# Kernel optimization log

Measured on AMD Instinct MI355X. Metric: run time of the kernel, lower is better.

## Reference

```python
import jax, jax.numpy as jnp
import numpy as np

B, R, A, L, P = 1024, 512, 196, 2, 4  # batch, rnn_size, att_size, num_layers, num_parallels


def setup_inputs() -> dict:
    key = jax.random.key(0)
    ks = jax.random.split(key, 24)
    s = 0.02
    inp = {
        'x': jax.random.normal(ks[0], (B, R), jnp.float32),
        'att': jax.random.normal(ks[1], (B, A, R), jnp.float32),
        'inputs': jax.random.normal(ks[2], (2 * L, B, R), jnp.float32),
        # first attention block
        'Wa2a': jax.random.normal(ks[3], (A, R), jnp.float32) * s,
        'ba2a': jnp.zeros((A,), jnp.float32),
        'Wh2a': jax.random.normal(ks[4], (A, R), jnp.float32) * s,
        'bh2a': jnp.zeros((A,), jnp.float32),
        'Wd2d': jax.random.normal(ks[5], (1, A), jnp.float32) * s,
        'bd2d': jnp.zeros((1,), jnp.float32),
        # second attention block
        'Wa2a1': jax.random.normal(ks[6], (A, R), jnp.float32) * s,
        'ba2a1': jnp.zeros((A,), jnp.float32),
        'Wh2a1': jax.random.normal(ks[7], (A, R), jnp.float32) * s,
        'bh2a1': jnp.zeros((A,), jnp.float32),
        'Wd2d1': jax.random.normal(ks[8], (1, A), jnp.float32) * s,
        'bd2d1': jnp.zeros((1,), jnp.float32),
        # per-parallel LSTM gate linears, stacked over P
        'Wi2h': jax.random.normal(ks[9], (P, 4 * R, R), jnp.float32) * s,
        'bi2h': jnp.zeros((P, 4 * R), jnp.float32),
        'Wh2h': jax.random.normal(ks[10], (P, 4 * R, R), jnp.float32) * s,
        'bh2h': jnp.zeros((P, 4 * R), jnp.float32),
        'Wa2h': jax.random.normal(ks[11], (P, 4 * R, R), jnp.float32) * s,
        'ba2h': jnp.zeros((P, 4 * R), jnp.float32),
    }
    return inp


def _attend(att, h, Wa, ba, Wh, bh, Wd, bd):
    # att: [B, S, R] with S == A (code requires it); h: [B, R]
    av = jnp.einsum('bsr,ar->bsa', att, Wa) + ba            # [B, S, A]
    ah = h @ Wh.T + bh                                      # [B, A]
    # original expands h-projection along the LAST axis (unsqueeze(2).expand)
    dot = jnp.tanh(av + ah[:, :, None])                     # [B, S, A]
    score = jnp.einsum('bsa,a->bs', dot, Wd[0]) + bd[0]     # [B, S]
    w = jax.nn.softmax(score, axis=-1)
    return jnp.einsum('bsr,bs->br', att, w)                 # [B, R]


def reference(x, att, inputs, Wa2a, ba2a, Wh2a, bh2a, Wd2d, bd2d,
              Wa2a1, ba2a1, Wh2a1, bh2a1, Wd2d1, bd2d1,
              Wi2h, bi2h, Wh2h, bh2h, Wa2h, ba2h):
    R_ = x.shape[-1]
    L_ = inputs.shape[0] // 2
    outputs = []
    for i in range(L_):
        prev_c = inputs[2 * i]
        prev_h = inputs[2 * i + 1]
        xt = x if i == 0 else x + outputs[-1]
        att_res = _attend(att, prev_h, Wa2a, ba2a, Wh2a, bh2a, Wd2d, bd2d)
        # stacked per-parallel gate sums: [P, B, 4R]
        sums = (jnp.einsum('bd,pgd->pbg', xt, Wi2h) + bi2h[:, None, :]
                + jnp.einsum('bd,pgd->pbg', prev_h, Wh2h) + bh2h[:, None, :]
                + jnp.einsum('bd,pgd->pbg', att_res, Wa2h) + ba2h[:, None, :])
        ig = jax.nn.sigmoid(sums[..., :R_])
        fg = jax.nn.sigmoid(sums[..., R_:2 * R_])
        og = jax.nn.sigmoid(sums[..., 2 * R_:3 * R_])
        it = jnp.tanh(sums[..., 3 * R_:])
        nc = fg * prev_c[None] + ig * it                    # [P, B, R]
        next_c = nc.mean(axis=0)
        next_h = (og * jnp.tanh(nc)).mean(axis=0)
        att_res1 = _attend(att, next_h, Wa2a1, ba2a1, Wh2a1, bh2a1, Wd2d1, bd2d1)
        top_h = att_res1 + next_h
        outputs.append(next_c)
        outputs.append(top_h)
    return jnp.stack(outputs)  # [2L, B, R]
```

## Files before the change

kernel.cpp:

```cpp
#include <hip/hip_runtime.h>
#include <math.h>

typedef __attribute__((ext_vector_type(8))) unsigned short ushort8_t;
typedef __attribute__((ext_vector_type(8))) short bf16x8;
typedef __attribute__((ext_vector_type(4))) float f32x4;

namespace {

constexpr int Bn = 1024;
constexpr int Rn = 512;
constexpr int An = 196;
constexpr int Gn = 8192;
constexpr int Kcat = 1536;
constexpr int NP = 224;
constexpr long ROWS = (long)Bn * An;

__device__ __forceinline__ float b2f(unsigned short u) {
  union { unsigned int i; float f; } v; v.i = ((unsigned int)u) << 16; return v.f;
}
__device__ __forceinline__ unsigned short f2b(float f) {
  union { float f; unsigned int i; } v; v.f = f;
  unsigned int r = v.i + 0x7fffu + ((v.i >> 16) & 1u);
  return (unsigned short)(r >> 16);
}
__device__ __forceinline__ float sigmf(float x) {
  return __builtin_amdgcn_rcpf(1.f + __expf(-x));
}
__device__ __forceinline__ float tanhf_fast(float x) {
  const float e = __expf(2.f * x);
  return 1.f - 2.f * __builtin_amdgcn_rcpf(e + 1.f);
}

__global__ __launch_bounds__(256)
void f2b_copy(const float* __restrict__ src, unsigned short* __restrict__ dst, long n)
{
  long i = ((long)blockIdx.x * 256 + threadIdx.x) * 8;
  const long stride = (long)gridDim.x * 256 * 8;
  for (; i + 8 <= n; i += stride) {
    float4 a = *(const float4*)(src + i);
    float4 b = *(const float4*)(src + i + 4);
    ushort8_t o;
    o[0] = f2b(a.x); o[1] = f2b(a.y); o[2] = f2b(a.z); o[3] = f2b(a.w);
    o[4] = f2b(b.x); o[5] = f2b(b.y); o[6] = f2b(b.z); o[7] = f2b(b.w);
    *(ushort8_t*)(dst + i) = o;
  }
}

__global__ __launch_bounds__(256)
void pack_wpad(const float* __restrict__ Wa0, const float* __restrict__ Wa1,
               unsigned short* __restrict__ Wp)
{
  long i = ((long)blockIdx.x * 256 + threadIdx.x) * 8;
  if (i >= 2L * NP * 512) return;
  const int set = (int)(i / (NP * 512));
  const int rem = (int)(i % (NP * 512));
  const int row = rem / 512, k = rem % 512;
  ushort8_t o;
  if (row < An) {
    const float* s = (set ? Wa1 : Wa0) + (long)row * 512 + k;
    float4 a = *(const float4*)s, b = *(const float4*)(s + 4);
    o[0] = f2b(a.x); o[1] = f2b(a.y); o[2] = f2b(a.z); o[3] = f2b(a.w);
    o[4] = f2b(b.x); o[5] = f2b(b.y); o[6] = f2b(b.z); o[7] = f2b(b.w);
  } else {
    o = ushort8_t{0,0,0,0,0,0,0,0};
  }
  *(ushort8_t*)(Wp + i) = o;
}

__global__ __launch_bounds__(256)
void pack_w(const float* __restrict__ Wi, const float* __restrict__ Wh,
            const float* __restrict__ Wa, unsigned short* __restrict__ W2)
{
  long i = ((long)blockIdx.x * 256 + threadIdx.x) * 8;
  if (i >= (long)Gn * Kcat) return;
  const int g = (int)(i / Kcat);
  const int k = (int)(i % Kcat);
  const float* src = (k < 512) ? Wi + (long)g * 512 + k
                   : (k < 1024) ? Wh + (long)g * 512 + (k - 512)
                   : Wa + (long)g * 512 + (k - 1024);
  float4 a = *(const float4*)src;
  float4 b = *(const float4*)(src + 4);
  ushort8_t o;
  o[0] = f2b(a.x); o[1] = f2b(a.y); o[2] = f2b(a.z); o[3] = f2b(a.w);
  o[4] = f2b(b.x); o[5] = f2b(b.y); o[6] = f2b(b.z); o[7] = f2b(b.w);
  *(ushort8_t*)(W2 + i) = o;
}

__global__ __launch_bounds__(256)
void pack_x(const float* __restrict__ xa, const float* __restrict__ xb,
            const float* __restrict__ h, const float* __restrict__ a,
            unsigned short* __restrict__ X2)
{
  long i = ((long)blockIdx.x * 256 + threadIdx.x) * 8;
  if (i >= (long)Bn * Kcat) return;
  const int b = (int)(i / Kcat);
  const int k = (int)(i % Kcat);
  ushort8_t o;
  if (k < 512) {
    const float* s = xa + (long)b * 512 + k;
    float4 v0 = *(const float4*)s, v1 = *(const float4*)(s + 4);
    if (xb) {
      const float* s2 = xb + (long)b * 512 + k;
      float4 w0 = *(const float4*)s2, w1 = *(const float4*)(s2 + 4);
      v0.x += w0.x; v0.y += w0.y; v0.z += w0.z; v0.w += w0.w;
      v1.x += w1.x; v1.y += w1.y; v1.z += w1.z; v1.w += w1.w;
    }
    o[0] = f2b(v0.x); o[1] = f2b(v0.y); o[2] = f2b(v0.z); o[3] = f2b(v0.w);
    o[4] = f2b(v1.x); o[5] = f2b(v1.y); o[6] = f2b(v1.z); o[7] = f2b(v1.w);
  } else {
    const float* s = (k < 1024) ? h + (long)b * 512 + (k - 512)
                                : a + (long)b * 512 + (k - 1024);
    float4 v0 = *(const float4*)s, v1 = *(const float4*)(s + 4);
    o[0] = f2b(v0.x); o[1] = f2b(v0.y); o[2] = f2b(v0.z); o[3] = f2b(v0.w);
    o[4] = f2b(v1.x); o[5] = f2b(v1.y); o[6] = f2b(v1.z); o[7] = f2b(v1.w);
  }
  *(ushort8_t*)(X2 + i) = o;
}

__global__ __launch_bounds__(512, 4)
void av_cs(const unsigned short* __restrict__ A,
           const unsigned short* __restrict__ Wpad,
           const float* __restrict__ b0vec, const float* __restrict__ b1vec,
           const float* __restrict__ Wd,
           const float* __restrict__ ah0, const float* __restrict__ ah1,
           float* __restrict__ s0, float* __restrict__ s1,
           unsigned short* __restrict__ av_out)
{
  __shared__ unsigned short As[128 * 32];
  __shared__ unsigned short Bs[224 * 32];
  __shared__ float wds[NP], bas[NP];
  __shared__ float ahAs[128], ahBs[128];
  __shared__ float sbA[128], sbB[128];

  const int tid = threadIdx.x;
  const int lane = tid & 63, w = tid >> 6;
  const int wr = w >> 1, wc = w & 1;
  const int fr = lane & 15, q = lane >> 4;
  const long row0 = (long)blockIdx.x * 128;
  const int set = blockIdx.y;

  if (set == 0) {
    if (tid < NP) {
      wds[tid] = (tid < An) ? Wd[tid] : 0.f;
      bas[tid] = (tid < An) ? b0vec[tid] : 0.f;
    }
    if (tid >= 256 && tid < 384) ahAs[tid - 256] = ah0[row0 + tid - 256];
    if (tid >= 384)              ahBs[tid - 384] = ah1[row0 + tid - 384];
  } else {
    if (tid < NP) bas[tid] = (tid < An) ? b1vec[tid] : 0.f;
  }

  const unsigned short* Ab = A + row0 * 512;
  const unsigned short* Bb = Wpad + (long)set * NP * 512;

  f32x4 acc[2][7] = {};

  const int grow = lane >> 2;
  const int gchk = (lane & 3) * 8;

  for (int kt = 0; kt < 512; kt += 32) {
    {
      const unsigned short* src = Ab + (long)(w * 16 + grow) * 512 + gchk + kt;
      __builtin_amdgcn_global_load_lds(
          (const __attribute__((address_space(1))) unsigned int*)src,
          (__attribute__((address_space(3))) unsigned int*)(As + w * 512), 16, 0, 0);
    }
    {
      const unsigned short* src = Bb + (long)(w * 16 + grow) * 512 + gchk + kt;
      __builtin_amdgcn_global_load_lds(
          (const __attribute__((address_space(1))) unsigned int*)src,
          (__attribute__((address_space(3))) unsigned int*)(Bs + w * 512), 16, 0, 0);
    }
    if (w < 6) {
      const unsigned short* src = Bb + (long)((w + 8) * 16 + grow) * 512 + gchk + kt;
      __builtin_amdgcn_global_load_lds(
          (const __attribute__((address_space(1))) unsigned int*)src,
          (__attribute__((address_space(3))) unsigned int*)(Bs + (w + 8) * 512), 16, 0, 0);
    }
    __syncthreads();
    bf16x8 af[2], bfr[7];
#pragma unroll
    for (int m = 0; m < 2; ++m)
      af[m] = *(const bf16x8*)&As[(wr * 32 + m * 16 + fr) * 32 + q * 8];
#pragma unroll
    for (int n = 0; n < 7; ++n)
      bfr[n] = *(const bf16x8*)&Bs[(wc * 112 + n * 16 + fr) * 32 + q * 8];
#pragma unroll
    for (int m = 0; m < 2; ++m)
#pragma unroll
      for (int n = 0; n < 7; ++n)
        acc[m][n] = __builtin_amdgcn_mfma_f32_16x16x32_bf16(af[m], bfr[n], acc[m][n], 0, 0, 0);
    __syncthreads();
  }

  if (set == 0) {
    float pA[2][4], pB[2][4];
#pragma unroll
    for (int m = 0; m < 2; ++m)
#pragma unroll
      for (int j = 0; j < 4; ++j) { pA[m][j] = 0.f; pB[m][j] = 0.f; }
#pragma unroll
    for (int n = 0; n < 7; ++n) {
      const int col = wc * 112 + n * 16 + fr;
      const float wd = wds[col];
      const float bv = bas[col];
#pragma unroll
      for (int m = 0; m < 2; ++m) {
#pragma unroll
        for (int j = 0; j < 4; ++j) {
          const int rl = wr * 32 + m * 16 + q * 4 + j;
          const float av = acc[m][n][j] + bv;
          pA[m][j] += wd * tanhf_fast(av + ahAs[rl]);
          pB[m][j] += wd * tanhf_fast(av + ahBs[rl]);
        }
      }
    }
#pragma unroll
    for (int m = 0; m < 2; ++m)
#pragma unroll
      for (int j = 0; j < 4; ++j) {
#pragma unroll
        for (int off = 1; off < 16; off <<= 1) {
          pA[m][j] += __shfl_xor(pA[m][j], off);
          pB[m][j] += __shfl_xor(pB[m][j], off);
        }
      }
    __syncthreads();
    if (wc == 0 && fr == 0) {
#pragma unroll
      for (int m = 0; m < 2; ++m)
#pragma unroll
        for (int j = 0; j < 4; ++j) {
          const int rl = wr * 32 + m * 16 + q * 4 + j;
          sbA[rl] = pA[m][j]; sbB[rl] = pB[m][j];
        }
    }
    __syncthreads();
    if (wc == 1 && fr == 0) {
#pragma unroll
      for (int m = 0; m < 2; ++m)
#pragma unroll
        for (int j = 0; j < 4; ++j) {
          const int rl = wr * 32 + m * 16 + q * 4 + j;
          sbA[rl] += pA[m][j]; sbB[rl] += pB[m][j];
        }
    }
    __syncthreads();
    if (tid < 128) {
      s0[row0 + tid] = sbA[tid];
      s1[row0 + tid] = sbB[tid];
    }
  } else {
#pragma unroll
    for (int n = 0; n < 7; ++n) {
      const int col = wc * 112 + n * 16 + fr;
      if (col >= An) continue;
      const float bv = bas[col];
#pragma unroll
      for (int m = 0; m < 2; ++m) {
#pragma unroll
        for (int j = 0; j < 4; ++j) {
          const long row = row0 + wr * 32 + m * 16 + q * 4 + j;
          av_out[row * An + col] = f2b(acc[m][n][j] + bv);
        }
      }
    }
  }
}

__global__ __launch_bounds__(256)
void gemm_gate(const unsigned short* __restrict__ A, const unsigned short* __restrict__ Bm,
               const float* __restrict__ bias, float* __restrict__ C)
{
  __shared__ unsigned short As[128 * 32];
  __shared__ unsigned short Bs[128 * 32];
  const int tid = threadIdx.x;
  const int lane = tid & 63, w = tid >> 6;
  int bid = blockIdx.x;
  bid = (bid & 7) * (gridDim.x >> 3) + (bid >> 3);
  const int bx = bid & 63;
  const int by = bid >> 6;
  const long row0 = (long)by * 128;
  const long col0 = (long)bx * 128;
  const int wr = w >> 1, wc = w & 1;
  const int fr = lane & 15, q = lane >> 4;
  const int srow = lane >> 2, schk = lane & 3;

  f32x4 acc[4][4] = {};
  const unsigned short* A0 = A + row0 * Kcat + schk * 8;
  const unsigned short* B0 = Bm + col0 * Kcat + schk * 8;

  for (int kt = 0; kt < Kcat; kt += 32) {
#pragma unroll
    for (int i = 0; i < 2; ++i) {
      const int rr = (w * 2 + i) * 16 + srow;
      __builtin_amdgcn_global_load_lds(
          (const __attribute__((address_space(1))) unsigned int*)(A0 + (long)rr * Kcat + kt),
          (__attribute__((address_space(3))) unsigned int*)(As + (w * 2 + i) * 512),
          16, 0, 0);
      __builtin_amdgcn_global_load_lds(
          (const __attribute__((address_space(1))) unsigned int*)(B0 + (long)rr * Kcat + kt),
          (__attribute__((address_space(3))) unsigned int*)(Bs + (w * 2 + i) * 512),
          16, 0, 0);
    }
    __syncthreads();
    bf16x8 af[4], bfr[4];
#pragma unroll
    for (int m = 0; m < 4; ++m)
      af[m] = *(const bf16x8*)&As[(wr * 64 + m * 16 + fr) * 32 + q * 8];
#pragma unroll
    for (int n = 0; n < 4; ++n)
      bfr[n] = *(const bf16x8*)&Bs[(wc * 64 + n * 16 + fr) * 32 + q * 8];
#pragma unroll
    for (int m = 0; m < 4; ++m)
#pragma unroll
      for (int n = 0; n < 4; ++n)
        acc[m][n] = __builtin_amdgcn_mfma_f32_16x16x32_bf16(af[m], bfr[n], acc[m][n], 0, 0, 0);
    __syncthreads();
  }

  const int crow = wr * 64 + q * 4;
  const int ccol = wc * 64 + fr;
#pragma unroll
  for (int n = 0; n < 4; ++n) {
    const int col = (int)col0 + ccol + n * 16;
    const float bv = bias[col];
#pragma unroll
    for (int m = 0; m < 4; ++m) {
      const long rb = row0 + crow + m * 16;
#pragma unroll
      for (int j = 0; j < 4; ++j)
        C[(rb + j) * (long)Gn + col] = acc[m][n][j] + bv;
    }
  }
}

__global__ __launch_bounds__(256)
void gemm_bf(const unsigned short* __restrict__ A, const unsigned short* __restrict__ Bm,
             const float* __restrict__ bias, float* __restrict__ C,
             int N, int K, int ldc)
{
  constexpr int LDP = 56;
  __shared__ unsigned short As[128 * LDP];
  __shared__ unsigned short Bs[128 * LDP];
  const int tid = threadIdx.x;
  const long row0 = (long)blockIdx.y * 128;
  const int col0 = blockIdx.x * 128;
  const int wid = tid >> 6, lane = tid & 63;
  const int wr = wid >> 1, wc = wid & 1;
  const int fr = lane & 15, kg = (lane >> 4) * 8;

  f32x4 acc[4][4] = {};

  const int srow = tid >> 1;
  const int skh = tid & 1;
  const unsigned short* Ap = A + (row0 + srow) * (long)K + skh * 16;
  const int bcol = col0 + srow;
  const unsigned short* Bp = Bm + (long)(bcol < N ? bcol : N - 1) * K + skh * 16;

  ushort8_t a0 = *(const ushort8_t*)(Ap);
  ushort8_t a1 = *(const ushort8_t*)(Ap + 8);
  ushort8_t b0 = *(const ushort8_t*)(Bp);
  ushort8_t b1 = *(const ushort8_t*)(Bp + 8);

  const int sw = srow * LDP + skh * 16;
  for (int kt = 0; kt < K; kt += 32) {
    *(ushort8_t*)&As[sw] = a0;
    *(ushort8_t*)&As[sw + 8] = a1;
    *(ushort8_t*)&Bs[sw] = b0;
    *(ushort8_t*)&Bs[sw + 8] = b1;
    if (kt + 32 < K) {
      a0 = *(const ushort8_t*)(Ap + kt + 32);
      a1 = *(const ushort8_t*)(Ap + kt + 40);
      b0 = *(const ushort8_t*)(Bp + kt + 32);
      b1 = *(const ushort8_t*)(Bp + kt + 40);
    }
    __syncthreads();
    bf16x8 af[4], bfr[4];
#pragma unroll
    for (int m = 0; m < 4; ++m)
      af[m] = *(const bf16x8*)&As[(wr * 64 + m * 16 + fr) * LDP + kg];
#pragma unroll
    for (int n = 0; n < 4; ++n)
      bfr[n] = *(const bf16x8*)&Bs[(wc * 64 + n * 16 + fr) * LDP + kg];
#pragma unroll
    for (int m = 0; m < 4; ++m)
#pragma unroll
      for (int n = 0; n < 4; ++n)
        acc[m][n] = __builtin_amdgcn_mfma_f32_16x16x32_bf16(af[m], bfr[n], acc[m][n], 0, 0, 0);
    __syncthreads();
  }

  const int crow = wr * 64 + (lane >> 4) * 4;
  const int ccol = wc * 64 + fr;
#pragma unroll
  for (int n = 0; n < 4; ++n) {
    const int col = col0 + ccol + n * 16;
    if (col >= N) continue;
    const float bv = bias ? bias[col] : 0.f;
#pragma unroll
    for (int m = 0; m < 4; ++m) {
      const long rb = row0 + crow + m * 16;
#pragma unroll
      for (int j = 0; j < 4; ++j)
        C[(rb + j) * (long)ldc + col] = acc[m][n][j] + bv;
    }
  }
}

__global__ __launch_bounds__(256)
void score1(const unsigned short* __restrict__ av, const float* __restrict__ ah,
            const float* __restrict__ Wd, float* __restrict__ s0)
{
  const int row = blockIdx.x * 4 + (threadIdx.x >> 6);
  const int lane = threadIdx.x & 63;
  const unsigned short* avp = av + (long)row * An;
  const float A0 = ah[row];
  float v0 = 0.f;
  for (int a = lane; a < An; a += 64)
    v0 += Wd[a] * tanhf_fast(b2f(avp[a]) + A0);
#pragma unroll
  for (int o = 32; o; o >>= 1) v0 += __shfl_down(v0, o);
  if (lane == 0) s0[row] = v0;
}

template<bool DUAL>
__global__ __launch_bounds__(256)
void wsum2(const unsigned short* __restrict__ att,
           const float* __restrict__ w0, const float* __restrict__ w1,
           const float* __restrict__ add0,
           float* __restrict__ o0, float* __restrict__ o1)
{
  const int half = threadIdx.x >> 7;
  const int b = blockIdx.x * 2 + half;
  const int t = threadIdx.x & 127;
  const int wv = t >> 6;
  __shared__ float ws0[2][An], ws1[2][An];
  __shared__ float redm[2][2][2], redsum[2][2][2];

  const float r0a = w0[(long)b * An + t];
  const float r0b = (t + 128 < An) ? w0[(long)b * An + t + 128] : -3.0e38f;
  float r1a = -3.0e38f, r1b = -3.0e38f;
  if (DUAL) {
    r1a = w1[(long)b * An + t];
    r1b = (t + 128 < An) ? w1[(long)b * An + t + 128] : -3.0e38f;
  }
  float m0 = fmaxf(r0a, r0b), m1 = fmaxf(r1a, r1b);
#pragma unroll
  for (int o = 32; o; o >>= 1) {
    m0 = fmaxf(m0, __shfl_xor(m0, o));
    if (DUAL) m1 = fmaxf(m1, __shfl_xor(m1, o));
  }
  if ((t & 63) == 0) { redm[0][half][wv] = m0; if (DUAL) redm[1][half][wv] = m1; }
  __syncthreads();
  m0 = fmaxf(redm[0][half][0], redm[0][half][1]);
  if (DUAL) m1 = fmaxf(redm[1][half][0], redm[1][half][1]);
  const float e0a = __expf(r0a - m0);
  const float e0b = (t + 128 < An) ? __expf(r0b - m0) : 0.f;
  float sl0 = e0a + e0b, sl1 = 0.f;
  float e1a = 0.f, e1b = 0.f;
  if (DUAL) {
    e1a = __expf(r1a - m1);
    e1b = (t + 128 < An) ? __expf(r1b - m1) : 0.f;
    sl1 = e1a + e1b;
  }
#pragma unroll
  for (int o = 32; o; o >>= 1) {
    sl0 += __shfl_xor(sl0, o);
    if (DUAL) sl1 += __shfl_xor(sl1, o);
  }
  if ((t & 63) == 0) { redsum[0][half][wv] = sl0; if (DUAL) redsum[1][half][wv] = sl1; }
  __syncthreads();
  const float inv0 = __builtin_amdgcn_rcpf(redsum[0][half][0] + redsum[0][half][1]);
  ws0[half][t] = e0a * inv0;
  if (t + 128 < An) ws0[half][t + 128] = e0b * inv0;
  if (DUAL) {
    const float inv1 = __builtin_amdgcn_rcpf(redsum[1][half][0] + redsum[1][half][1]);
    ws1[half][t] = e1a * inv1;
    if (t + 128 < An) ws1[half][t + 128] = e1b * inv1;
  }
  __syncthreads();

  const unsigned short* ap = att + (long)b * An * Rn + t * 4;
  float a00 = 0, a01 = 0, a02 = 0, a03 = 0;
  float a10 = 0, a11 = 0, a12 = 0, a13 = 0;
  for (int s = 0; s < An; ++s) {
    ushort4 u = *(const ushort4*)(ap + (long)s * Rn);
    const float f0 = b2f(u.x), f1 = b2f(u.y), f2 = b2f(u.z), f3 = b2f(u.w);
    const float v0 = ws0[half][s];
    a00 = fmaf(f0, v0, a00); a01 = fmaf(f1, v0, a01);
    a02 = fmaf(f2, v0, a02); a03 = fmaf(f3, v0, a03);
    if (DUAL) {
      const float v1 = ws1[half][s];
      a10 = fmaf(f0, v1, a10); a11 = fmaf(f1, v1, a11);
      a12 = fmaf(f2, v1, a12); a13 = fmaf(f3, v1, a13);
    }
  }
  const long base = (long)b * Rn + t * 4;
  if (add0) {
    float4 ad = *(const float4*)(add0 + base);
    a00 += ad.x; a01 += ad.y; a02 += ad.z; a03 += ad.w;
  }
  *(float4*)(o0 + base) = make_float4(a00, a01, a02, a03);
  if (DUAL) *(float4*)(o1 + base) = make_float4(a10, a11, a12, a13);
}

__global__ __launch_bounds__(256)
void gates_pw(const float* __restrict__ sums, const float* __restrict__ prev_c,
              float* __restrict__ out_c, float* __restrict__ nh,
              unsigned short* __restrict__ nh_bf)
{
  const int i = blockIdx.x * 256 + threadIdx.x;
  const int b = i >> 9;
  const int r = i & 511;
  const float c = prev_c[i];
  float aC = 0.f, aH = 0.f;
#pragma unroll
  for (int p = 0; p < 4; ++p) {
    const float* sp = sums + (long)b * Gn + p * 2048 + r;
    const float ig = sigmf(sp[0]);
    const float fg = sigmf(sp[512]);
    const float og = sigmf(sp[1024]);
    const float it = tanhf_fast(sp[1536]);
    const float nc = fmaf(fg, c, ig * it);
    aC += nc;
    aH = fmaf(og, tanhf_fast(nc), aH);
  }
  out_c[i] = aC * 0.25f;
  const float hv = aH * 0.25f;
  nh[i] = hv;
  nh_bf[i] = f2b(hv);
}

__global__ __launch_bounds__(256)
void bias3(const float* __restrict__ a, const float* __restrict__ b,
           const float* __restrict__ c, float* __restrict__ o, int n)
{
  const int i = blockIdx.x * 256 + threadIdx.x;
  if (i < n) o[i] = a[i] + b[i] + c[i];
}

}

extern "C" void kernel_launch(void* const* d_in, const int* in_sizes, int n_in,
                              void* d_out, int out_size, void* d_ws, size_t ws_size,
                              hipStream_t stream)
{
  const float* x      = (const float*)d_in[0];
  const float* att    = (const float*)d_in[1];
  const float* inputs = (const float*)d_in[2];
  const float* Wa2a   = (const float*)d_in[3];
  const float* ba2a   = (const float*)d_in[4];
  const float* Wh2a   = (const float*)d_in[5];
  const float* bh2a   = (const float*)d_in[6];
  const float* Wd2d   = (const float*)d_in[7];
  const float* Wa2a1  = (const float*)d_in[9];
  const float* ba2a1  = (const float*)d_in[10];
  const float* Wh2a1  = (const float*)d_in[11];
  const float* bh2a1  = (const float*)d_in[12];
  const float* Wd2d1  = (const float*)d_in[13];
  const float* Wi2h   = (const float*)d_in[15];
  const float* bi2h   = (const float*)d_in[16];
  const float* Wh2h   = (const float*)d_in[17];
  const float* bh2h   = (const float*)d_in[18];
  const float* Wa2h   = (const float*)d_in[19];
  const float* ba2h   = (const float*)d_in[20];
  (void)in_sizes; (void)n_in; (void)out_size; (void)ws_size;

  float* out = (float*)d_out;
  const float* prev_c0 = inputs + 0 * (long)Bn * Rn;
  const float* prev_h0 = inputs + 1 * (long)Bn * Rn;
  const float* prev_c1 = inputs + 2 * (long)Bn * Rn;
  const float* prev_h1 = inputs + 3 * (long)Bn * Rn;

  char* wsp = (char*)d_ws;
  size_t off = 0;
  auto alloc = [&](size_t bytes) -> void* {
    void* p = wsp + off;
    off += (bytes + 1023) & ~(size_t)1023;
    return p;
  };
  unsigned short* att_bf  = (unsigned short*)alloc(ROWS * Rn * 2);
  unsigned short* W2      = (unsigned short*)alloc((size_t)Gn * Kcat * 2);
  unsigned short* Wpad    = (unsigned short*)alloc((size_t)2 * NP * Rn * 2);
  unsigned short* wh2a_bf = (unsigned short*)alloc((size_t)An * Rn * 2);
  unsigned short* wh2a1_bf= (unsigned short*)alloc((size_t)An * Rn * 2);
  unsigned short* h01_bf  = (unsigned short*)alloc((size_t)2 * Bn * Rn * 2);
  unsigned short* nh_bf   = (unsigned short*)alloc((size_t)Bn * Rn * 2);
  unsigned short* X2      = (unsigned short*)alloc((size_t)Bn * Kcat * 2);
  unsigned short* av1_bf  = (unsigned short*)alloc(ROWS * An * 2);
  float* ahAB = (float*)alloc((size_t)2 * ROWS * 4);
  float* ah1  = (float*)alloc(ROWS * 4);
  float* scA  = (float*)alloc(ROWS * 4);
  float* scB  = (float*)alloc(ROWS * 4);
  float* sc1  = (float*)alloc(ROWS * 4);
  float* res0 = (float*)alloc((size_t)Bn * Rn * 4);
  float* res1 = (float*)alloc((size_t)Bn * Rn * 4);
  float* nh   = (float*)alloc((size_t)Bn * Rn * 4);
  float* bsum = (float*)alloc((size_t)Gn * 4);
  float* sums = (float*)alloc((size_t)Bn * Gn * 4);

  float* ahA = ahAB;
  float* ahB = ahAB + ROWS;

  const dim3 blk(256);

  f2b_copy<<<dim3(50176), blk, 0, stream>>>(att, att_bf, ROWS * Rn);
  pack_wpad<<<dim3(112), blk, 0, stream>>>(Wa2a, Wa2a1, Wpad);
  f2b_copy<<<dim3(49), blk, 0, stream>>>(Wh2a,  wh2a_bf,  (long)An * Rn);
  f2b_copy<<<dim3(49), blk, 0, stream>>>(Wh2a1, wh2a1_bf, (long)An * Rn);
  f2b_copy<<<dim3(256), blk, 0, stream>>>(prev_h0, h01_bf, (long)Bn * Rn);
  f2b_copy<<<dim3(256), blk, 0, stream>>>(prev_h1, h01_bf + (long)Bn * Rn, (long)Bn * Rn);
  pack_w<<<dim3(6144), blk, 0, stream>>>(Wi2h, Wh2h, Wa2h, W2);
  bias3<<<dim3(Gn / 256), blk, 0, stream>>>(bi2h, bh2h, ba2h, bsum, Gn);

  gemm_bf<<<dim3(2, 16), blk, 0, stream>>>(h01_bf, wh2a_bf, bh2a, ahA, An, Rn, An);

  av_cs<<<dim3((int)(ROWS / 128), 2), dim3(512), 0, stream>>>(
      att_bf, Wpad, ba2a, ba2a1, Wd2d, ahA, ahB, scA, scB, av1_bf);
  wsum2<true><<<dim3(Bn / 2), blk, 0, stream>>>(att_bf, scA, scB, (const float*)nullptr, res0, res1);

  pack_x<<<dim3(768), blk, 0, stream>>>(x, (const float*)nullptr, prev_h0, res0, X2);
  gemm_gate<<<dim3(512), blk, 0, stream>>>(X2, W2, bsum, sums);
  gates_pw<<<dim3(Bn * Rn / 256), blk, 0, stream>>>(sums, prev_c0, out + 0, nh, nh_bf);

  gemm_bf<<<dim3(2, Bn / 128), blk, 0, stream>>>(nh_bf, wh2a1_bf, bh2a1, ah1, An, Rn, An);
  score1<<<dim3((int)(ROWS / 4)), blk, 0, stream>>>(av1_bf, ah1, Wd2d1, sc1);
  wsum2<false><<<dim3(Bn / 2), blk, 0, stream>>>(att_bf, sc1, (const float*)nullptr, nh,
                                                 out + (long)Bn * Rn, (float*)nullptr);

  pack_x<<<dim3(768), blk, 0, stream>>>(x, out + (long)Bn * Rn, prev_h1, res1, X2);
  gemm_gate<<<dim3(512), blk, 0, stream>>>(X2, W2, bsum, sums);
  gates_pw<<<dim3(Bn * Rn / 256), blk, 0, stream>>>(sums, prev_c1, out + 2 * (long)Bn * Rn, nh, nh_bf);

  gemm_bf<<<dim3(2, Bn / 128), blk, 0, stream>>>(nh_bf, wh2a1_bf, bh2a1, ah1, An, Rn, An);
  score1<<<dim3((int)(ROWS / 4)), blk, 0, stream>>>(av1_bf, ah1, Wd2d1, sc1);
  wsum2<false><<<dim3(Bn / 2), blk, 0, stream>>>(att_bf, sc1, (const float*)nullptr, nh,
                                                 out + 3 * (long)Bn * Rn, (float*)nullptr);
}
```

Before: 714.5 us.

## Fuse small pack kernels and write attention results directly into bf16 GEMM inputs

After: 655.0 us. 8.3% less time.

```diff
diff --git a/kernel.cpp b/kernel.cpp
--- a/kernel.cpp
+++ b/kernel.cpp
@@ -47,24 +47,50 @@
 }
 
 __global__ __launch_bounds__(256)
-void pack_wpad(const float* __restrict__ Wa0, const float* __restrict__ Wa1,
-               unsigned short* __restrict__ Wp)
-{
-  long i = ((long)blockIdx.x * 256 + threadIdx.x) * 8;
-  if (i >= 2L * NP * 512) return;
-  const int set = (int)(i / (NP * 512));
-  const int rem = (int)(i % (NP * 512));
-  const int row = rem / 512, k = rem % 512;
-  ushort8_t o;
-  if (row < An) {
-    const float* s = (set ? Wa1 : Wa0) + (long)row * 512 + k;
-    float4 a = *(const float4*)s, b = *(const float4*)(s + 4);
-    o[0] = f2b(a.x); o[1] = f2b(a.y); o[2] = f2b(a.z); o[3] = f2b(a.w);
-    o[4] = f2b(b.x); o[5] = f2b(b.y); o[6] = f2b(b.z); o[7] = f2b(b.w);
+void pack_small(const float* __restrict__ Wa0, const float* __restrict__ Wa1,
+                const float* __restrict__ Wh0, const float* __restrict__ Wh1,
+                const float* __restrict__ inputs,
+                unsigned short* __restrict__ Wp, unsigned short* __restrict__ whcat,
+                unsigned short* __restrict__ h01)
+{
+  const int blk = blockIdx.x;
+  if (blk < 112) {
+    long i = ((long)blk * 256 + threadIdx.x) * 8;
+    if (i >= 2L * NP * 512) return;
+    const int set = (int)(i / (NP * 512));
+    const int rem = (int)(i % (NP * 512));
+    const int row = rem / 512, k = rem % 512;
+    ushort8_t o;
+    if (row < An) {
+      const float* s = (set ? Wa1 : Wa0) + (long)row * 512 + k;
+      float4 a = *(const float4*)s, b = *(const float4*)(s + 4);
+      o[0] = f2b(a.x); o[1] = f2b(a.y); o[2] = f2b(a.z); o[3] = f2b(a.w);
+      o[4] = f2b(b.x); o[5] = f2b(b.y); o[6] = f2b(b.z); o[7] = f2b(b.w);
+    } else {
+      o = ushort8_t{0,0,0,0,0,0,0,0};
+    }
+    *(ushort8_t*)(Wp + i) = o;
+  } else if (blk < 210) {
+    long i = ((long)(blk - 112) * 256 + threadIdx.x) * 8;
+    if (i >= 2L * An * 512) return;
+    const long half = (long)An * 512;
+    const float* s = (i < half) ? Wh0 + i : Wh1 + (i - half);
+    float4 v0 = *(const float4*)s, v1 = *(const float4*)(s + 4);
+    ushort8_t o;
+    o[0] = f2b(v0.x); o[1] = f2b(v0.y); o[2] = f2b(v0.z); o[3] = f2b(v0.w);
+    o[4] = f2b(v1.x); o[5] = f2b(v1.y); o[6] = f2b(v1.z); o[7] = f2b(v1.w);
+    *(ushort8_t*)(whcat + i) = o;
   } else {
-    o = ushort8_t{0,0,0,0,0,0,0,0};
-  }
-  *(ushort8_t*)(Wp + i) = o;
+    long i = ((long)(blk - 210) * 256 + threadIdx.x) * 8;
+    if (i >= 2L * Bn * 512) return;
+    const long half = (long)Bn * 512;
+    const float* s = (i < half) ? inputs + half + i : inputs + 3 * half + (i - half);
+    float4 v0 = *(const float4*)s, v1 = *(const float4*)(s + 4);
+    ushort8_t o;
+    o[0] = f2b(v0.x); o[1] = f2b(v0.y); o[2] = f2b(v0.z); o[3] = f2b(v0.w);
+    o[4] = f2b(v1.x); o[5] = f2b(v1.y); o[6] = f2b(v1.z); o[7] = f2b(v1.w);
+    *(ushort8_t*)(h01 + i) = o;
+  }
 }
 
 __global__ __launch_bounds__(256)
@@ -87,34 +113,23 @@
 }
 
 __global__ __launch_bounds__(256)
-void pack_x(const float* __restrict__ xa, const float* __restrict__ xb,
-            const float* __restrict__ h, const float* __restrict__ a,
-            unsigned short* __restrict__ X2)
+void pack_sec3(const float* __restrict__ x, const float* __restrict__ h0,
+               const float* __restrict__ h1,
+               unsigned short* __restrict__ X20, unsigned short* __restrict__ X21)
 {
   long i = ((long)blockIdx.x * 256 + threadIdx.x) * 8;
-  if (i >= (long)Bn * Kcat) return;
-  const int b = (int)(i / Kcat);
-  const int k = (int)(i % Kcat);
+  if (i >= 3L * Bn * 512) return;
+  const int sec = (int)(i / ((long)Bn * 512));
+  const long r = i % ((long)Bn * 512);
+  const int b = (int)(r >> 9);
+  const int k = (int)(r & 511);
+  const float* src = (sec == 0 ? x : sec == 1 ? h0 : h1) + r;
+  unsigned short* dst = (sec == 2 ? X21 : X20) + (long)b * Kcat + (sec ? 512 : 0) + k;
+  float4 v0 = *(const float4*)src, v1 = *(const float4*)(src + 4);
   ushort8_t o;
-  if (k < 512) {
-    const float* s = xa + (long)b * 512 + k;
-    float4 v0 = *(const float4*)s, v1 = *(const float4*)(s + 4);
-    if (xb) {
-      const float* s2 = xb + (long)b * 512 + k;
-      float4 w0 = *(const float4*)s2, w1 = *(const float4*)(s2 + 4);
-      v0.x += w0.x; v0.y += w0.y; v0.z += w0.z; v0.w += w0.w;
-      v1.x += w1.x; v1.y += w1.y; v1.z += w1.z; v1.w += w1.w;
-    }
-    o[0] = f2b(v0.x); o[1] = f2b(v0.y); o[2] = f2b(v0.z); o[3] = f2b(v0.w);
-    o[4] = f2b(v1.x); o[5] = f2b(v1.y); o[6] = f2b(v1.z); o[7] = f2b(v1.w);
-  } else {
-    const float* s = (k < 1024) ? h + (long)b * 512 + (k - 512)
-                                : a + (long)b * 512 + (k - 1024);
-    float4 v0 = *(const float4*)s, v1 = *(const float4*)(s + 4);
-    o[0] = f2b(v0.x); o[1] = f2b(v0.y); o[2] = f2b(v0.z); o[3] = f2b(v0.w);
-    o[4] = f2b(v1.x); o[5] = f2b(v1.y); o[6] = f2b(v1.z); o[7] = f2b(v1.w);
-  }
-  *(ushort8_t*)(X2 + i) = o;
+  o[0] = f2b(v0.x); o[1] = f2b(v0.y); o[2] = f2b(v0.z); o[3] = f2b(v0.w);
+  o[4] = f2b(v1.x); o[5] = f2b(v1.y); o[6] = f2b(v1.z); o[7] = f2b(v1.w);
+  *(ushort8_t*)dst = o;
 }
 
 __global__ __launch_bounds__(512, 4)
@@ -270,7 +285,8 @@
 
 __global__ __launch_bounds__(256)
 void gemm_gate(const unsigned short* __restrict__ A, const unsigned short* __restrict__ Bm,
-               const float* __restrict__ bias, float* __restrict__ C)
+               const float* __restrict__ b1, const float* __restrict__ b2,
+               const float* __restrict__ b3, float* __restrict__ C)
 {
   __shared__ unsigned short As[128 * 32];
   __shared__ unsigned short Bs[128 * 32];
@@ -324,7 +340,7 @@
 #pragma unroll
   for (int n = 0; n < 4; ++n) {
     const int col = (int)col0 + ccol + n * 16;
-    const float bv = bias[col];
+    const float bv = b1[col] + b2[col] + b3[col];
 #pragma unroll
     for (int m = 0; m < 4; ++m) {
       const long rb = row0 + crow + m * 16;
@@ -414,22 +430,23 @@
 {
   const int row = blockIdx.x * 4 + (threadIdx.x >> 6);
   const int lane = threadIdx.x & 63;
-  const unsigned short* avp = av + (long)row * An;
   const float A0 = ah[row];
   float v0 = 0.f;
-  for (int a = lane; a < An; a += 64)
-    v0 += Wd[a] * tanhf_fast(b2f(avp[a]) + A0);
+  if (lane < 49) {
+    ushort4 u = *(const ushort4*)(av + (long)row * An + lane * 4);
+    float4 w = *(const float4*)(Wd + lane * 4);
+    v0 = w.x * tanhf_fast(b2f(u.x) + A0) + w.y * tanhf_fast(b2f(u.y) + A0)
+       + w.z * tanhf_fast(b2f(u.z) + A0) + w.w * tanhf_fast(b2f(u.w) + A0);
+  }
 #pragma unroll
   for (int o = 32; o; o >>= 1) v0 += __shfl_down(v0, o);
   if (lane == 0) s0[row] = v0;
 }
 
-template<bool DUAL>
-__global__ __launch_bounds__(256)
-void wsum2(const unsigned short* __restrict__ att,
-           const float* __restrict__ w0, const float* __restrict__ w1,
-           const float* __restrict__ add0,
-           float* __restrict__ o0, float* __restrict__ o1)
+__global__ __launch_bounds__(256)
+void wsumA(const unsigned short* __restrict__ att,
+           const float* __restrict__ scA, const float* __restrict__ scB,
+           unsigned short* __restrict__ X20, unsigned short* __restrict__ X21)
 {
   const int half = threadIdx.x >> 7;
   const int b = blockIdx.x * 2 + half;
@@ -438,46 +455,39 @@
   __shared__ float ws0[2][An], ws1[2][An];
   __shared__ float redm[2][2][2], redsum[2][2][2];
 
-  const float r0a = w0[(long)b * An + t];
-  const float r0b = (t + 128 < An) ? w0[(long)b * An + t + 128] : -3.0e38f;
-  float r1a = -3.0e38f, r1b = -3.0e38f;
-  if (DUAL) {
-    r1a = w1[(long)b * An + t];
-    r1b = (t + 128 < An) ? w1[(long)b * An + t + 128] : -3.0e38f;
-  }
+  const float r0a = scA[(long)b * An + t];
+  const float r0b = (t + 128 < An) ? scA[(long)b * An + t + 128] : -3.0e38f;
+  const float r1a = scB[(long)b * An + t];
+  const float r1b = (t + 128 < An) ? scB[(long)b * An + t + 128] : -3.0e38f;
   float m0 = fmaxf(r0a, r0b), m1 = fmaxf(r1a, r1b);
 #pragma unroll
   for (int o = 32; o; o >>= 1) {
     m0 = fmaxf(m0, __shfl_xor(m0, o));
-    if (DUAL) m1 = fmaxf(m1, __shfl_xor(m1, o));
-  }
-  if ((t & 63) == 0) { redm[0][half][wv] = m0; if (DUAL) redm[1][half][wv] = m1; }
+    m1 = fmaxf(m1, __shfl_xor(m1, o));
+  }
+  if ((t & 63) == 0) { redm[0][half][wv] = m0; redm[1][half][wv] = m1; }
   __syncthreads();
   m0 = fmaxf(redm[0][half][0], redm[0][half][1]);
-  if (DUAL) m1 = fmaxf(redm[1][half][0], redm[1][half][1]);
+  m1 = fmaxf(redm[1][half][0], redm[1][half][1]);
   const float e0a = __expf(r0a - m0);
   const float e0b = (t + 128 < An) ? __expf(r0b - m0) : 0.f;
-  float sl0 = e0a + e0b, sl1 = 0.f;
-  float e1a = 0.f, e1b = 0.f;
-  if (DUAL) {
-    e1a = __expf(r1a - m1);
-    e1b = (t + 128 < An) ? __expf(r1b - m1) : 0.f;
-    sl1 = e1a + e1b;
-  }
+  const float e1a = __expf(r1a - m1);
+  const float e1b = (t + 128 < An) ? __expf(r1b - m1) : 0.f;
+  float sl0 = e0a + e0b, sl1 = e1a + e1b;
 #pragma unroll
   for (int o = 32; o; o >>= 1) {
     sl0 += __shfl_xor(sl0, o);
-    if (DUAL) sl1 += __shfl_xor(sl1, o);
-  }
-  if ((t & 63) == 0) { redsum[0][half][wv] = sl0; if (DUAL) redsum[1][half][wv] = sl1; }
+    sl1 += __shfl_xor(sl1, o);
+  }
+  if ((t & 63) == 0) { redsum[0][half][wv] = sl0; redsum[1][half][wv] = sl1; }
   __syncthreads();
   const float inv0 = __builtin_amdgcn_rcpf(redsum[0][half][0] + redsum[0][half][1]);
+  const float inv1 = __builtin_amdgcn_rcpf(redsum[1][half][0] + redsum[1][half][1]);
   ws0[half][t] = e0a * inv0;
-  if (t + 128 < An) ws0[half][t + 128] = e0b * inv0;
-  if (DUAL) {
-    const float inv1 = __builtin_amdgcn_rcpf(redsum[1][half][0] + redsum[1][half][1]);
-    ws1[half][t] = e1a * inv1;
-    if (t + 128 < An) ws1[half][t + 128] = e1b * inv1;
+  ws1[half][t] = e1a * inv1;
+  if (t + 128 < An) {
+    ws0[half][t + 128] = e0b * inv0;
+    ws1[half][t + 128] = e1b * inv1;
   }
   __syncthreads();
 
@@ -490,19 +500,71 @@
     const float v0 = ws0[half][s];
     a00 = fmaf(f0, v0, a00); a01 = fmaf(f1, v0, a01);
     a02 = fmaf(f2, v0, a02); a03 = fmaf(f3, v0, a03);
-    if (DUAL) {
-      const float v1 = ws1[half][s];
-      a10 = fmaf(f0, v1, a10); a11 = fmaf(f1, v1, a11);
-      a12 = fmaf(f2, v1, a12); a13 = fmaf(f3, v1, a13);
-    }
+    const float v1 = ws1[half][s];
+    a10 = fmaf(f0, v1, a10); a11 = fmaf(f1, v1, a11);
+    a12 = fmaf(f2, v1, a12); a13 = fmaf(f3, v1, a13);
+  }
+  const long base = (long)b * Kcat + 1024 + t * 4;
+  ushort4 oA, oB;
+  oA.x = f2b(a00); oA.y = f2b(a01); oA.z = f2b(a02); oA.w = f2b(a03);
+  oB.x = f2b(a10); oB.y = f2b(a11); oB.z = f2b(a12); oB.w = f2b(a13);
+  *(ushort4*)(X20 + base) = oA;
+  *(ushort4*)(X21 + base) = oB;
+}
+
+template<bool WX2>
+__global__ __launch_bounds__(256)
+void wsumB(const unsigned short* __restrict__ att,
+           const float* __restrict__ sc, const float* __restrict__ nh,
+           const float* __restrict__ xin,
+           float* __restrict__ outp, unsigned short* __restrict__ X21)
+{
+  const int half = threadIdx.x >> 7;
+  const int b = blockIdx.x * 2 + half;
+  const int t = threadIdx.x & 127;
+  const int wv = t >> 6;
+  __shared__ float ws[2][An];
+  __shared__ float redm[2][2], redsum[2][2];
+
+  const float ra = sc[(long)b * An + t];
+  const float rb = (t + 128 < An) ? sc[(long)b * An + t + 128] : -3.0e38f;
+  float m0 = fmaxf(ra, rb);
+#pragma unroll
+  for (int o = 32; o; o >>= 1) m0 = fmaxf(m0, __shfl_xor(m0, o));
+  if ((t & 63) == 0) redm[half][wv] = m0;
+  __syncthreads();
+  m0 = fmaxf(redm[half][0], redm[half][1]);
+  const float ea = __expf(ra - m0);
+  const float eb = (t + 128 < An) ? __expf(rb - m0) : 0.f;
+  float sl = ea + eb;
+#pragma unroll
+  for (int o = 32; o; o >>= 1) sl += __shfl_xor(sl, o);
+  if ((t & 63) == 0) redsum[half][wv] = sl;
+  __syncthreads();
+  const float inv = __builtin_amdgcn_rcpf(redsum[half][0] + redsum[half][1]);
+  ws[half][t] = ea * inv;
+  if (t + 128 < An) ws[half][t + 128] = eb * inv;
+  __syncthreads();
+
+  const unsigned short* ap = att + (long)b * An * Rn + t * 4;
+  float a0 = 0, a1 = 0, a2 = 0, a3 = 0;
+  for (int s = 0; s < An; ++s) {
+    ushort4 u = *(const ushort4*)(ap + (long)s * Rn);
+    const float w = ws[half][s];
+    a0 = fmaf(b2f(u.x), w, a0); a1 = fmaf(b2f(u.y), w, a1);
+    a2 = fmaf(b2f(u.z), w, a2); a3 = fmaf(b2f(u.w), w, a3);
   }
   const long base = (long)b * Rn + t * 4;
-  if (add0) {
-    float4 ad = *(const float4*)(add0 + base);
-    a00 += ad.x; a01 += ad.y; a02 += ad.z; a03 += ad.w;
-  }
-  *(float4*)(o0 + base) = make_float4(a00, a01, a02, a03);
-  if (DUAL) *(float4*)(o1 + base) = make_float4(a10, a11, a12, a13);
+  float4 ad = *(const float4*)(nh + base);
+  a0 += ad.x; a1 += ad.y; a2 += ad.z; a3 += ad.w;
+  *(float4*)(outp + base) = make_float4(a0, a1, a2, a3);
+  if (WX2) {
+    float4 xv = *(const float4*)(xin + base);
+    ushort4 o;
+    o.x = f2b(a0 + xv.x); o.y = f2b(a1 + xv.y);
+    o.z = f2b(a2 + xv.z); o.w = f2b(a3 + xv.w);
+    *(ushort4*)(X21 + (long)b * Kcat + t * 4) = o;
+  }
 }
 
 __global__ __launch_bounds__(256)
@@ -530,14 +592,6 @@
   const float hv = aH * 0.25f;
   nh[i] = hv;
   nh_bf[i] = f2b(hv);
-}
-
-__global__ __launch_bounds__(256)
-void bias3(const float* __restrict__ a, const float* __restrict__ b,
-           const float* __restrict__ c, float* __restrict__ o, int n)
-{
-  const int i = blockIdx.x * 256 + threadIdx.x;
-  if (i < n) o[i] = a[i] + b[i] + c[i];
 }
 
 }
@@ -583,58 +637,54 @@
   unsigned short* att_bf  = (unsigned short*)alloc(ROWS * Rn * 2);
   unsigned short* W2      = (unsigned short*)alloc((size_t)Gn * Kcat * 2);
   unsigned short* Wpad    = (unsigned short*)alloc((size_t)2 * NP * Rn * 2);
-  unsigned short* wh2a_bf = (unsigned short*)alloc((size_t)An * Rn * 2);
-  unsigned short* wh2a1_bf= (unsigned short*)alloc((size_t)An * Rn * 2);
+  unsigned short* whcat   = (unsigned short*)alloc((size_t)2 * An * Rn * 2);
   unsigned short* h01_bf  = (unsigned short*)alloc((size_t)2 * Bn * Rn * 2);
   unsigned short* nh_bf   = (unsigned short*)alloc((size_t)Bn * Rn * 2);
-  unsigned short* X2      = (unsigned short*)alloc((size_t)Bn * Kcat * 2);
+  unsigned short* X20     = (unsigned short*)alloc((size_t)Bn * Kcat * 2);
+  unsigned short* X21     = (unsigned short*)alloc((size_t)Bn * Kcat * 2);
   unsigned short* av1_bf  = (unsigned short*)alloc(ROWS * An * 2);
   float* ahAB = (float*)alloc((size_t)2 * ROWS * 4);
   float* ah1  = (float*)alloc(ROWS * 4);
   float* scA  = (float*)alloc(ROWS * 4);
   float* scB  = (float*)alloc(ROWS * 4);
   float* sc1  = (float*)alloc(ROWS * 4);
-  float* res0 = (float*)alloc((size_t)Bn * Rn * 4);
-  float* res1 = (float*)alloc((size_t)Bn * Rn * 4);
   float* nh   = (float*)alloc((size_t)Bn * Rn * 4);
-  float* bsum = (float*)alloc((size_t)Gn * 4);
   float* sums = (float*)alloc((size_t)Bn * Gn * 4);
 
   float* ahA = ahAB;
   float* ahB = ahAB + ROWS;
+  unsigned short* wh2a_bf  = whcat;
+  unsigned short* wh2a1_bf = whcat + (size_t)An * Rn;
 
   const dim3 blk(256);
 
   f2b_copy<<<dim3(50176), blk, 0, stream>>>(att, att_bf, ROWS * Rn);
-  pack_wpad<<<dim3(112), blk, 0, stream>>>(Wa2a, Wa2a1, Wpad);
-  f2b_copy<<<dim3(49), blk, 0, stream>>>(Wh2a,  wh2a_bf,  (long)An * Rn);
-  f2b_copy<<<dim3(49), blk, 0, stream>>>(Wh2a1, wh2a1_bf, (long)An * Rn);
-  f2b_copy<<<dim3(256), blk, 0, stream>>>(prev_h0, h01_bf, (long)Bn * Rn);
-  f2b_copy<<<dim3(256), blk, 0, stream>>>(prev_h1, h01_bf + (long)Bn * Rn, (long)Bn * Rn);
+  pack_small<<<dim3(722), blk, 0, stream>>>(Wa2a, Wa2a1, Wh2a, Wh2a1, inputs,
+                                            Wpad, whcat, h01_bf);
   pack_w<<<dim3(6144), blk, 0, stream>>>(Wi2h, Wh2h, Wa2h, W2);
-  bias3<<<dim3(Gn / 256), blk, 0, stream>>>(bi2h, bh2h, ba2h, bsum, Gn);
+  pack_sec3<<<dim3(768), blk, 0, stream>>>(x, prev_h0, prev_h1, X20, X21);
 
   gemm_bf<<<dim3(2, 16), blk, 0, stream>>>(h01_bf, wh2a_bf, bh2a, ahA, An, Rn, An);
 
   av_cs<<<dim3((int)(ROWS / 128), 2), dim3(512), 0, stream>>>(
       att_bf, Wpad, ba2a, ba2a1, Wd2d, ahA, ahB, scA, scB, av1_bf);
-  wsum2<true><<<dim3(Bn / 2), blk, 0, stream>>>(att_bf, scA, scB, (const float*)nullptr, res0, res1);
-
-  pack_x<<<dim3(768), blk, 0, stream>>>(x, (const float*)nullptr, prev_h0, res0, X2);
-  gemm_gate<<<dim3(512), blk, 0, stream>>>(X2, W2, bsum, sums);
+
+  wsumA<<<dim3(Bn / 2), blk, 0, stream>>>(att_bf, scA, scB, X20, X21);
+
+  gemm_gate<<<dim3(512), blk, 0, stream>>>(X20, W2, bi2h, bh2h, ba2h, sums);
   gates_pw<<<dim3(Bn * Rn / 256), blk, 0, stream>>>(sums, prev_c0, out + 0, nh, nh_bf);
 
   gemm_bf<<<dim3(2, Bn / 128), blk, 0, stream>>>(nh_bf, wh2a1_bf, bh2a1, ah1, An, Rn, An);
   score1<<<dim3((int)(ROWS / 4)), blk, 0, stream>>>(av1_bf, ah1, Wd2d1, sc1);
-  wsum2<false><<<dim3(Bn / 2), blk, 0, stream>>>(att_bf, sc1, (const float*)nullptr, nh,
-                                                 out + (long)Bn * Rn, (float*)nullptr);
-
-  pack_x<<<dim3(768), blk, 0, stream>>>(x, out + (long)Bn * Rn, prev_h1, res1, X2);
-  gemm_gate<<<dim3(512), blk, 0, stream>>>(X2, W2, bsum, sums);
+  wsumB<true><<<dim3(Bn / 2), blk, 0, stream>>>(att_bf, sc1, nh, x,
+                                                out + (long)Bn * Rn, X21);
+
+  gemm_gate<<<dim3(512), blk, 0, stream>>>(X21, W2, bi2h, bh2h, ba2h, sums);
   gates_pw<<<dim3(Bn * Rn / 256), blk, 0, stream>>>(sums, prev_c1, out + 2 * (long)Bn * Rn, nh, nh_bf);
 
   gemm_bf<<<dim3(2, Bn / 128), blk, 0, stream>>>(nh_bf, wh2a1_bf, bh2a1, ah1, An, Rn, An);
   score1<<<dim3((int)(ROWS / 4)), blk, 0, stream>>>(av1_bf, ah1, Wd2d1, sc1);
-  wsum2<false><<<dim3(Bn / 2), blk, 0, stream>>>(att_bf, sc1, (const float*)nullptr, nh,
-                                                 out + 3 * (long)Bn * Rn, (float*)nullptr);
-}
+  wsumB<false><<<dim3(Bn / 2), blk, 0, stream>>>(att_bf, sc1, nh, (const float*)nullptr,
+                                                 out + 3 * (long)Bn * Rn,
+                                                 (unsigned short*)nullptr);
+}
```
